# Optimization experiments

Hardware: AMD Instinct MI355X
Metric: run time of the kernel (lower is better)

The kernel has to match this reference:

```python
import jax, jax.numpy as jnp
import numpy as np

N_NODES = 100000
N_EDGES = 1600000
N_GRAPHS = 512


def gcn_conv(x, W, b, src, dst, n_nodes):
    """GCNConv with self-loops: D^-1/2 (A+I) D^-1/2 X W + b."""
    h = x @ W  # [N, out]
    ones = jnp.ones((src.shape[0],), h.dtype)
    deg = jax.ops.segment_sum(ones, dst, num_segments=n_nodes) + 1.0  # +1 self-loop
    dinv = jax.lax.rsqrt(deg)
    norm = dinv[src] * dinv[dst]  # [E]
    agg = jax.ops.segment_sum(h[src] * norm[:, None], dst, num_segments=n_nodes)
    agg = agg + h * (1.0 / deg)[:, None]  # self-loop term: deg^-0.5 * deg^-0.5
    return agg + b


def setup_inputs() -> dict:
    key = jax.random.key(0)
    ks = jax.random.split(key, 12)
    x = jax.random.normal(ks[0], (N_NODES, 78), dtype=jnp.float32)
    edge_index = jax.random.randint(ks[1], (2, N_EDGES), 0, N_NODES, dtype=jnp.int64)
    batch = jnp.sort(jax.random.randint(ks[2], (N_NODES,), 0, N_GRAPHS, dtype=jnp.int64))
    def glorot(k, shape):
        lim = np.sqrt(6.0 / (shape[0] + shape[1])).astype(np.float32)
        return jax.random.uniform(k, shape, jnp.float32, -lim, lim)
    return {
        "x": x,
        "edge_index": edge_index,
        "batch": batch,
        "W1": glorot(ks[3], (78, 128)),
        "b1": jnp.zeros((128,), jnp.float32),
        "W2": glorot(ks[4], (128, 256)),
        "b2": jnp.zeros((256,), jnp.float32),
        "Wg1": glorot(ks[5], (256, 1024)),
        "bg1": jnp.zeros((1024,), jnp.float32),
        "Wg2": glorot(ks[6], (1024, 128)),
        "bg2": jnp.zeros((128,), jnp.float32),
    }


def reference(x, edge_index, batch, W1, b1, W2, b2, Wg1, bg1, Wg2, bg2):
    src, dst = edge_index[0], edge_index[1]
    n = x.shape[0]
    h = jax.nn.relu(gcn_conv(x, W1, b1, src, dst, n))   # [N,128]
    h = jax.nn.relu(gcn_conv(h, W2, b2, src, dst, n))   # [N,256]
    g = jax.ops.segment_max(h, batch, num_segments=N_GRAPHS)  # global max pool [G,256]
    g = jax.nn.relu(g @ Wg1 + bg1)   # [G,1024]; dropout is identity at eval
    g = g @ Wg2 + bg2                # [G,128]
    return g
```

## Files before the change

kernel.cpp:

```cpp
#include <hip/hip_runtime.h>
#include <hip/hip_fp16.h>


#define NN 100000
#define NE 1600000
#define NG 512
#define NBLK ((NN + 1023) / 1024)

typedef float v2f __attribute__((ext_vector_type(2)));
typedef _Float16 half8 __attribute__((ext_vector_type(8)));
typedef float f32x4 __attribute__((ext_vector_type(4)));


__global__ void k_hist(const int* __restrict__ dst, int* cnt, int e) {
    int i = blockIdx.x * blockDim.x + threadIdx.x;
    if (i < e) atomicAdd(&cnt[dst[i]], 1);
}

__global__ void k_prep(const int* __restrict__ cnt, float* __restrict__ dinv,
                       float* __restrict__ gmax) {
    int i = blockIdx.x * blockDim.x + threadIdx.x;
    if (i < NN) dinv[i] = rsqrtf((float)cnt[i] + 1.0f);
    if (i < NG * 256) gmax[i] = 0.0f;
}

__global__ void k_cvt_x(const float* __restrict__ x, __half* __restrict__ xh) {
    int i = blockIdx.x * blockDim.x + threadIdx.x;
    if (i < NN * 39) {
        float2 v = ((const float2*)x)[i];
        ((__half2*)xh)[i] = __floats2half2_rn(v.x, v.y);
    }
}

__global__ void k_pack_w2(const float* __restrict__ W, __half* __restrict__ Wh,
                          __half* __restrict__ Wl) {
    int i = blockIdx.x * blockDim.x + threadIdx.x;
    if (i >= 32768) return;
    int j = i & 7, lane = (i >> 3) & 63, ks = (i >> 9) & 3, nt = i >> 11;
    int n = nt * 16 + (lane & 15);
    int k = ks * 32 + ((lane >> 4) << 3) + j;
    float v = W[k * 256 + n];
    __half hi = __float2half_rn(v);
    Wh[i] = hi;
    Wl[i] = __float2half_rn(v - __half2float(hi));
}

__global__ __launch_bounds__(256) void k_bsum(const int* __restrict__ cnt, int* __restrict__ bsum) {
    __shared__ int s[256];
    int b = blockIdx.x, t = threadIdx.x;
    int base = b * 1024 + t * 4;
    int v = 0;
#pragma unroll
    for (int j = 0; j < 4; j++) { int i = base + j; if (i < NN) v += cnt[i]; }
    s[t] = v; __syncthreads();
    for (int off = 128; off > 0; off >>= 1) {
        if (t < off) s[t] += s[t + off];
        __syncthreads();
    }
    if (t == 0) bsum[b] = s[0];
}

__global__ __launch_bounds__(128) void k_scan_bsum(int* bsum, int* row_ptr) {
    __shared__ int s[128];
    int t = threadIdx.x;
    int v = (t < NBLK) ? bsum[t] : 0;
    s[t] = v; __syncthreads();
    for (int off = 1; off < 128; off <<= 1) {
        int u = (t >= off) ? s[t - off] : 0;
        __syncthreads();
        s[t] += u;
        __syncthreads();
    }
    if (t < NBLK) bsum[t] = s[t] - v;
    if (t == 0) row_ptr[NN] = NE;
}

__global__ __launch_bounds__(256) void k_scan_blocks(const int* __restrict__ cnt,
    const int* __restrict__ bsum, int* __restrict__ row_ptr, int* __restrict__ cursor) {
    __shared__ int s[256];
    int b = blockIdx.x, t = threadIdx.x;
    int base = b * 1024 + t * 4;
    int v[4]; int sum = 0;
#pragma unroll
    for (int j = 0; j < 4; j++) { int i = base + j; v[j] = (i < NN) ? cnt[i] : 0; sum += v[j]; }
    s[t] = sum; __syncthreads();
    for (int off = 1; off < 256; off <<= 1) {
        int u = (t >= off) ? s[t - off] : 0;
        __syncthreads();
        s[t] += u;
        __syncthreads();
    }
    int excl = s[t] - sum + bsum[b];
#pragma unroll
    for (int j = 0; j < 4; j++) {
        int i = base + j;
        if (i < NN) { row_ptr[i] = excl; cursor[i] = excl; excl += v[j]; }
    }
}

__global__ void k_fillslots(const int* __restrict__ src, const int* __restrict__ dst,
    const float* __restrict__ dinv, int* cursor, int2* __restrict__ es, int e) {
    int i = blockIdx.x * blockDim.x + threadIdx.x;
    if (i >= e) return;
    int s = src[i], d = dst[i];
    int pos = atomicAdd(&cursor[d], 1);
    es[pos] = make_int2(s, __float_as_int(dinv[s] * dinv[d]));
}

__global__ __launch_bounds__(256) void k_fused1(const __half* __restrict__ x,
    const int* __restrict__ rp, const int2* __restrict__ es,
    const float* __restrict__ dinv, const float* __restrict__ W,
    const float* __restrict__ bias, __half* __restrict__ out) {
    __shared__ float As[4][8][80];
    int tid = threadIdx.x;
    int wv = tid >> 6, l = tid & 63;
    int task = __builtin_amdgcn_readfirstlane(blockIdx.x * 4 + wv);
    int n0 = task * 8;
    if (n0 >= NN) return;

    if (l < 39) {
        for (int pi = 0; pi < 4; pi++) {
            int nA = n0 + 2 * pi, nB = nA + 1;
            float diA = dinv[nA], swA = diA * diA;
            float diB = dinv[nB], swB = diB * diB;
            float2 aA = __half22float2(((const __half2*)(x + (size_t)nA * 78))[l]);
            float2 aB = __half22float2(((const __half2*)(x + (size_t)nB * 78))[l]);
            aA.x *= swA; aA.y *= swA;
            aB.x *= swB; aB.y *= swB;
            int eA = rp[nA], eA1 = rp[nA + 1];
            int eB = rp[nB], eB1 = rp[nB + 1];
            int cA = (eA1 - eA) >> 3, cB = (eB1 - eB) >> 3;
            while (cA > 0 || cB > 0) {
                bool dA = (cA > 0), dB = (cB > 0);
                int2 esA[8], esB[8];
                __half2 vA[8], vB[8];
                if (dA) {
#pragma unroll
                    for (int j = 0; j < 8; j++) esA[j] = es[eA + j];
                }
                if (dB) {
#pragma unroll
                    for (int j = 0; j < 8; j++) esB[j] = es[eB + j];
                }
                if (dA) {
#pragma unroll
                    for (int j = 0; j < 8; j++)
                        vA[j] = ((const __half2*)(x + (size_t)esA[j].x * 78))[l];
                }
                if (dB) {
#pragma unroll
                    for (int j = 0; j < 8; j++)
                        vB[j] = ((const __half2*)(x + (size_t)esB[j].x * 78))[l];
                }
                if (dA) {
#pragma unroll
                    for (int j = 0; j < 8; j++) {
                        float w = __int_as_float(esA[j].y);
                        float2 v = __half22float2(vA[j]);
                        aA.x += v.x * w; aA.y += v.y * w;
                    }
                    eA += 8; cA--;
                }
                if (dB) {
#pragma unroll
                    for (int j = 0; j < 8; j++) {
                        float w = __int_as_float(esB[j].y);
                        float2 v = __half22float2(vB[j]);
                        aB.x += v.x * w; aB.y += v.y * w;
                    }
                    eB += 8; cB--;
                }
            }
            while (eA < eA1 && eB < eB1) {
                int2 pA = es[eA], pB = es[eB];
                float2 vA2 = __half22float2(((const __half2*)(x + (size_t)pA.x * 78))[l]);
                float2 vB2 = __half22float2(((const __half2*)(x + (size_t)pB.x * 78))[l]);
                float wA = __int_as_float(pA.y), wB = __int_as_float(pB.y);
                aA.x += vA2.x * wA; aA.y += vA2.y * wA;
                aB.x += vB2.x * wB; aB.y += vB2.y * wB;
                eA++; eB++;
            }
            for (; eA < eA1; eA++) {
                int2 p = es[eA];
                float w = __int_as_float(p.y);
                float2 v = __half22float2(((const __half2*)(x + (size_t)p.x * 78))[l]);
                aA.x += v.x * w; aA.y += v.y * w;
            }
            for (; eB < eB1; eB++) {
                int2 p = es[eB];
                float w = __int_as_float(p.y);
                float2 v = __half22float2(((const __half2*)(x + (size_t)p.x * 78))[l]);
                aB.x += v.x * w; aB.y += v.y * w;
            }
            *(float2*)&As[wv][2 * pi][2 * l] = aA;
            *(float2*)&As[wv][2 * pi + 1][2 * l] = aB;
        }
    }

    int f0 = l * 2;
    float2 acc[8];
#pragma unroll
    for (int i = 0; i < 8; i++) acc[i] = make_float2(0.f, 0.f);

    for (int k = 0; k < 76; k += 4) {
        float2 w0 = *(const float2*)&W[(k + 0) * 128 + f0];
        float2 w1 = *(const float2*)&W[(k + 1) * 128 + f0];
        float2 w2 = *(const float2*)&W[(k + 2) * 128 + f0];
        float2 w3 = *(const float2*)&W[(k + 3) * 128 + f0];
#pragma unroll
        for (int i = 0; i < 8; i++) {
            float4 a = *(const float4*)&As[wv][i][k];
            acc[i].x += a.x * w0.x + a.y * w1.x + a.z * w2.x + a.w * w3.x;
            acc[i].y += a.x * w0.y + a.y * w1.y + a.z * w2.y + a.w * w3.y;
        }
    }
    {
        float2 w0 = *(const float2*)&W[76 * 128 + f0];
        float2 w1 = *(const float2*)&W[77 * 128 + f0];
#pragma unroll
        for (int i = 0; i < 8; i++) {
            float2 a = *(const float2*)&As[wv][i][76];
            acc[i].x += a.x * w0.x + a.y * w1.x;
            acc[i].y += a.x * w0.y + a.y * w1.y;
        }
    }
    float2 bv = *(const float2*)&bias[f0];
#pragma unroll
    for (int i = 0; i < 8; i++) {
        float ox = fmaxf(acc[i].x + bv.x, 0.f);
        float oy = fmaxf(acc[i].y + bv.y, 0.f);
        *(__half2*)&out[(size_t)(n0 + i) * 128 + f0] = __floats2half2_rn(ox, oy);
    }
}

__global__ __launch_bounds__(256) void k_fused2(const __half* __restrict__ h,
    const int* __restrict__ rp, const int2* __restrict__ es,
    const float* __restrict__ dinv, const __half* __restrict__ W2h,
    const __half* __restrict__ W2l, const float* __restrict__ bias,
    const int* __restrict__ batch, unsigned* __restrict__ gmax) {
    __shared__ __half As[4][16][128];
    int tid = threadIdx.x;
    int wv = tid >> 6, l = tid & 63;
    int task = __builtin_amdgcn_readfirstlane(blockIdx.x * 4 + wv);
    if (task >= 6250) return;
    int n0 = task * 16;

    char* lbase = (char*)&As[wv][0][0];
    int chunkw = (l >> 2);
    int subw = (l & 3) * 4;

    for (int pi = 0; pi < 8; pi++) {
        int nA = n0 + 2 * pi, nB = nA + 1;
        float diA = dinv[nA], swA = diA * diA;
        float diB = dinv[nB], swB = diB * diB;
        float2 aA = __half22float2(((const __half2*)(h + (size_t)nA * 128))[l]);
        float2 aB = __half22float2(((const __half2*)(h + (size_t)nB * 128))[l]);
        aA.x *= swA; aA.y *= swA;
        aB.x *= swB; aB.y *= swB;
        int eA = rp[nA], eA1 = rp[nA + 1];
        int eB = rp[nB], eB1 = rp[nB + 1];
        int cA = (eA1 - eA) >> 3, cB = (eB1 - eB) >> 3;
        while (cA > 0 || cB > 0) {
            bool dA = (cA > 0), dB = (cB > 0);
            int2 esA[8], esB[8];
            __half2 vA[8], vB[8];
            if (dA) {
#pragma unroll
                for (int j = 0; j < 8; j++) esA[j] = es[eA + j];
            }
            if (dB) {
#pragma unroll
                for (int j = 0; j < 8; j++) esB[j] = es[eB + j];
            }
            if (dA) {
#pragma unroll
                for (int j = 0; j < 8; j++)
                    vA[j] = ((const __half2*)(h + (size_t)esA[j].x * 128))[l];
            }
            if (dB) {
#pragma unroll
                for (int j = 0; j < 8; j++)
                    vB[j] = ((const __half2*)(h + (size_t)esB[j].x * 128))[l];
            }
            if (dA) {
#pragma unroll
                for (int j = 0; j < 8; j++) {
                    float w = __int_as_float(esA[j].y);
                    float2 v = __half22float2(vA[j]);
                    aA.x += v.x * w; aA.y += v.y * w;
                }
                eA += 8; cA--;
            }
            if (dB) {
#pragma unroll
                for (int j = 0; j < 8; j++) {
                    float w = __int_as_float(esB[j].y);
                    float2 v = __half22float2(vB[j]);
                    aB.x += v.x * w; aB.y += v.y * w;
                }
                eB += 8; cB--;
            }
        }
        while (eA < eA1 && eB < eB1) {
            int2 pA = es[eA], pB = es[eB];
            float2 vA2 = __half22float2(((const __half2*)(h + (size_t)pA.x * 128))[l]);
            float2 vB2 = __half22float2(((const __half2*)(h + (size_t)pB.x * 128))[l]);
            float wA = __int_as_float(pA.y), wB = __int_as_float(pB.y);
            aA.x += vA2.x * wA; aA.y += vA2.y * wA;
            aB.x += vB2.x * wB; aB.y += vB2.y * wB;
            eA++; eB++;
        }
        for (; eA < eA1; eA++) {
            int2 p = es[eA];
            float w = __int_as_float(p.y);
            float2 v = __half22float2(((const __half2*)(h + (size_t)p.x * 128))[l]);
            aA.x += v.x * w; aA.y += v.y * w;
        }
        for (; eB < eB1; eB++) {
            int2 p = es[eB];
            float w = __int_as_float(p.y);
            float2 v = __half22float2(((const __half2*)(h + (size_t)p.x * 128))[l]);
            aB.x += v.x * w; aB.y += v.y * w;
        }
        int rA = 2 * pi, rB = 2 * pi + 1;
        *(__half2*)(lbase + rA * 256 + ((chunkw ^ rA) << 4) + subw) =
            __floats2half2_rn(aA.x, aA.y);
        *(__half2*)(lbase + rB * 256 + ((chunkw ^ rB) << 4) + subw) =
            __floats2half2_rn(aB.x, aB.y);
    }

    int am = l & 15;
    int row4 = (l >> 4) << 2;
    int gg[4];
#pragma unroll
    for (int r = 0; r < 4; r++) gg[r] = batch[n0 + row4 + r];

    half8 ah[4];
#pragma unroll
    for (int ks = 0; ks < 4; ks++) {
        int c = ks * 4 + (l >> 4);
        ah[ks] = *(const half8*)(lbase + am * 256 + ((c ^ am) << 4));
    }

    for (int hh = 0; hh < 2; hh++) {
        f32x4 acc[8];
#pragma unroll
        for (int i = 0; i < 8; i++) acc[i] = (f32x4)(0.f);
#pragma unroll
        for (int ks = 0; ks < 4; ks++) {
#pragma unroll
            for (int nt = 0; nt < 8; nt++) {
                int fi = ((((hh * 8 + nt) * 4 + ks) * 64) + l) * 8;
                half8 bh = *(const half8*)&W2h[fi];
                half8 bl = *(const half8*)&W2l[fi];
                acc[nt] = __builtin_amdgcn_mfma_f32_16x16x32_f16(ah[ks], bh, acc[nt], 0, 0, 0);
                acc[nt] = __builtin_amdgcn_mfma_f32_16x16x32_f16(ah[ks], bl, acc[nt], 0, 0, 0);
            }
        }
#pragma unroll
        for (int nt = 0; nt < 8; nt++) {
            int n = (hh * 8 + nt) * 16 + am;
            float bv = bias[n];
            int curg = -1;
            float m = 0.f;
#pragma unroll
            for (int r = 0; r < 4; r++) {
                int g = gg[r];
                float v = fmaxf(acc[nt][r] + bv, 0.f);
                if (g != curg) {
                    if (curg >= 0) atomicMax(&gmax[(size_t)curg * 256 + n], __float_as_uint(m));
                    curg = g; m = v;
                } else {
                    m = fmaxf(m, v);
                }
            }
            if (curg >= 0) atomicMax(&gmax[(size_t)curg * 256 + n], __float_as_uint(m));
        }
    }
}


__global__ __launch_bounds__(256) void k_gemm3(const float* __restrict__ A,
    const float* __restrict__ W, const float* __restrict__ bias,
    float* __restrict__ out) {
    __shared__ float rs[8][256];
    int b = blockIdx.x, tid = threadIdx.x;
#pragma unroll
    for (int g = 0; g < 8; g++) rs[g][tid] = A[(b * 8 + g) * 256 + tid];
    __syncthreads();
    float acc[8][4];
#pragma unroll
    for (int g = 0; g < 8; g++)
#pragma unroll
        for (int j = 0; j < 4; j++) acc[g][j] = 0.f;
    for (int k = 0; k < 256; k++) {
        float w0 = W[k * 1024 + tid];
        float w1 = W[k * 1024 + tid + 256];
        float w2 = W[k * 1024 + tid + 512];
        float w3 = W[k * 1024 + tid + 768];
#pragma unroll
        for (int g = 0; g < 8; g++) {
            float a = rs[g][k];
            acc[g][0] += a * w0; acc[g][1] += a * w1;
            acc[g][2] += a * w2; acc[g][3] += a * w3;
        }
    }
#pragma unroll
    for (int g = 0; g < 8; g++)
#pragma unroll
        for (int j = 0; j < 4; j++) {
            int f = tid + j * 256;
            out[(b * 8 + g) * 1024 + f] = fmaxf(acc[g][j] + bias[f], 0.0f);
        }
}

__global__ __launch_bounds__(128) void k_gemm4(const float* __restrict__ A,
    const float* __restrict__ W, const float* __restrict__ bias,
    float* __restrict__ out) {
    __shared__ float rs[4][1024];
    int b = blockIdx.x, tid = threadIdx.x;
    for (int i = tid; i < 4096; i += 128) rs[i >> 10][i & 1023] = A[b * 4096 + i];
    __syncthreads();
    float acc[4] = {0.f, 0.f, 0.f, 0.f};
    for (int k = 0; k < 1024; k++) {
        float wv = W[k * 128 + tid];
#pragma unroll
        for (int g = 0; g < 4; g++) acc[g] += rs[g][k] * wv;
    }
#pragma unroll
    for (int g = 0; g < 4; g++)
        out[(b * 4 + g) * 128 + tid] = acc[g] + bias[tid];
}

extern "C" void kernel_launch(void* const* d_in, const int* in_sizes, int n_in,
                              void* d_out, int out_size, void* d_ws, size_t ws_size,
                              hipStream_t stream) {
    const float* x    = (const float*)d_in[0];
    const int*   ei   = (const int*)d_in[1];
    const int*   batch= (const int*)d_in[2];
    const float* W1   = (const float*)d_in[3];
    const float* b1   = (const float*)d_in[4];
    const float* W2   = (const float*)d_in[5];
    const float* b2   = (const float*)d_in[6];
    const float* Wg1  = (const float*)d_in[7];
    const float* bg1  = (const float*)d_in[8];
    const float* Wg2  = (const float*)d_in[9];
    const float* bg2  = (const float*)d_in[10];
    const int* src = ei;
    const int* dst = ei + NE;

    char* w8 = (char*)d_ws;
    int*   cnt     = (int*)w8;                 w8 += (size_t)NN * 4;
    int*   row_ptr = (int*)w8;                 w8 += (size_t)(NN + 4) * 4;
    int*   cursor  = (int*)w8;                 w8 += (size_t)NN * 4;
    int*   bsum    = (int*)w8;                 w8 += 128 * 4;
    int2*  es      = (int2*)w8;                w8 += (size_t)NE * 8;
    float* dinv    = (float*)w8;               w8 += (size_t)NN * 4;
    __half* xh     = (__half*)w8;              w8 += (size_t)NN * 78 * 2;
    __half* h1     = (__half*)w8;              w8 += (size_t)NN * 128 * 2;
    __half* w2h    = (__half*)w8;              w8 += 32768 * 2;
    __half* w2l    = (__half*)w8;              w8 += 32768 * 2;
    unsigned* gmax = (unsigned*)w8;            w8 += (size_t)NG * 256 * 4;
    float* g1      = (float*)w8;               w8 += (size_t)NG * 1024 * 4;

    hipMemsetAsync(cnt, 0, (size_t)NN * 4, stream);
    k_hist<<<(NE + 255) / 256, 256, 0, stream>>>(dst, cnt, NE);
    k_cvt_x<<<(NN * 39 + 255) / 256, 256, 0, stream>>>(x, xh);
    k_pack_w2<<<128, 256, 0, stream>>>(W2, w2h, w2l);
    k_prep<<<(NG * 256 + 255) / 256, 256, 0, stream>>>(cnt, dinv, (float*)gmax);
    k_bsum<<<NBLK, 256, 0, stream>>>(cnt, bsum);
    k_scan_bsum<<<1, 128, 0, stream>>>(bsum, row_ptr);
    k_scan_blocks<<<NBLK, 256, 0, stream>>>(cnt, bsum, row_ptr, cursor);
    k_fillslots<<<(NE + 255) / 256, 256, 0, stream>>>(src, dst, dinv, cursor, es, NE);

    k_fused1<<<NN / 32, 256, 0, stream>>>(xh, row_ptr, es, dinv, W1, b1, h1);

    k_fused2<<<(6250 + 3) / 4, 256, 0, stream>>>(h1, row_ptr, es, dinv, w2h, w2l, b2, batch, gmax);

    k_gemm3<<<NG / 8, 256, 0, stream>>>((const float*)gmax, Wg1, bg1, g1);
    k_gemm4<<<NG / 4, 128, 0, stream>>>(g1, Wg2, bg2, (float*)d_out);
}
```

Baseline: 591.1 us.

## Split layer-2 gather from MFMA pooling and degree-sort pairs in layer 1

Layer 2 is split into two kernels. The first gathers neighbour rows, one node per wavefront, with software-prefetched edge slots, and writes a half-precision aggregate buffer. The second runs the MFMA GEMM over 64-row tiles and does the max-pool epilogue. Separately, layer 1 sorts each wave's 8 nodes by degree so the paired nodes have similar edge counts, which reduces divergence in the dual-node loop. The split costs an extra write and read of a 100k x 128 half buffer. The MFMA tail tile reads padded rows of that buffer that were never written; those rows are masked out in the pooling step.

```diff
diff --git a/kernel.cpp b/kernel.cpp
--- a/kernel.cpp
+++ b/kernel.cpp
@@ -6,6 +6,8 @@
 #define NE 1600000
 #define NG 512
 #define NBLK ((NN + 1023) / 1024)
+#define NTASK2 1563
+#define NNPAD 100032
 
 typedef float v2f __attribute__((ext_vector_type(2)));
 typedef _Float16 half8 __attribute__((ext_vector_type(8)));
@@ -118,9 +120,28 @@
     int n0 = task * 8;
     if (n0 >= NN) return;
 
+    int deg[8], idx[8];
+    {
+        int e0 = rp[n0], ei;
+#pragma unroll
+        for (int i = 0; i < 8; i++) {
+            ei = rp[n0 + i + 1];
+            deg[i] = ei - e0; e0 = ei; idx[i] = i;
+        }
+    }
+#pragma unroll
+    for (int i = 1; i < 8; i++) {
+        int dv = deg[i], iv = idx[i], j = i - 1;
+        while (j >= 0 && deg[j] > dv) {
+            deg[j + 1] = deg[j]; idx[j + 1] = idx[j]; j--;
+        }
+        deg[j + 1] = dv; idx[j + 1] = iv;
+    }
+
     if (l < 39) {
         for (int pi = 0; pi < 4; pi++) {
-            int nA = n0 + 2 * pi, nB = nA + 1;
+            int iA = idx[2 * pi], iB = idx[2 * pi + 1];
+            int nA = n0 + iA, nB = n0 + iB;
             float diA = dinv[nA], swA = diA * diA;
             float diB = dinv[nB], swB = diB * diB;
             float2 aA = __half22float2(((const __half2*)(x + (size_t)nA * 78))[l]);
@@ -192,8 +213,8 @@
                 float2 v = __half22float2(((const __half2*)(x + (size_t)p.x * 78))[l]);
                 aB.x += v.x * w; aB.y += v.y * w;
             }
-            *(float2*)&As[wv][2 * pi][2 * l] = aA;
-            *(float2*)&As[wv][2 * pi + 1][2 * l] = aB;
+            *(float2*)&As[wv][iA][2 * l] = aA;
+            *(float2*)&As[wv][iB][2 * l] = aB;
         }
     }
 
@@ -233,148 +254,113 @@
     }
 }
 
-__global__ __launch_bounds__(256) void k_fused2(const __half* __restrict__ h,
+__global__ __launch_bounds__(256) void k_gather128h(const __half* __restrict__ h,
     const int* __restrict__ rp, const int2* __restrict__ es,
-    const float* __restrict__ dinv, const __half* __restrict__ W2h,
-    const __half* __restrict__ W2l, const float* __restrict__ bias,
-    const int* __restrict__ batch, unsigned* __restrict__ gmax) {
-    __shared__ __half As[4][16][128];
+    const float* __restrict__ dinv, __half* __restrict__ agg) {
+    int n = blockIdx.x * 4 + (threadIdx.x >> 6);
+    int l = threadIdx.x & 63;
+    float di = dinv[n], sw = di * di;
+    float2 a = __half22float2(((const __half2*)(h + (size_t)n * 128))[l]);
+    a.x *= sw; a.y *= sw;
+    int e = rp[n], e1 = rp[n + 1];
+    int nf = (e1 - e) >> 3;
+    if (nf > 0) {
+        int2 cur[8];
+#pragma unroll
+        for (int j = 0; j < 8; j++) cur[j] = es[e + j];
+        for (int b = 1; ; b++) {
+            __half2 v[8];
+#pragma unroll
+            for (int j = 0; j < 8; j++)
+                v[j] = ((const __half2*)(h + (size_t)cur[j].x * 128))[l];
+            e += 8;
+            bool more = (b < nf);
+            int2 nxt[8];
+            if (more) {
+#pragma unroll
+                for (int j = 0; j < 8; j++) nxt[j] = es[e + j];
+            }
+#pragma unroll
+            for (int j = 0; j < 8; j++) {
+                float w = __int_as_float(cur[j].y);
+                float2 vv = __half22float2(v[j]);
+                a.x += vv.x * w; a.y += vv.y * w;
+            }
+            if (!more) break;
+#pragma unroll
+            for (int j = 0; j < 8; j++) cur[j] = nxt[j];
+        }
+    }
+    for (; e < e1; e++) {
+        int2 p = es[e];
+        float w = __int_as_float(p.y);
+        float2 v = __half22float2(((const __half2*)(h + (size_t)p.x * 128))[l]);
+        a.x += v.x * w; a.y += v.y * w;
+    }
+    ((__half2*)(agg + (size_t)n * 128))[l] = __floats2half2_rn(a.x, a.y);
+}
+
+__global__ __launch_bounds__(256) void k_mm2pool(const __half* __restrict__ A,
+    const __half* __restrict__ W2h, const __half* __restrict__ W2l,
+    const float* __restrict__ bias, const int* __restrict__ batch,
+    unsigned* __restrict__ gmax) {
     int tid = threadIdx.x;
     int wv = tid >> 6, l = tid & 63;
     int task = __builtin_amdgcn_readfirstlane(blockIdx.x * 4 + wv);
-    if (task >= 6250) return;
-    int n0 = task * 16;
-
-    char* lbase = (char*)&As[wv][0][0];
-    int chunkw = (l >> 2);
-    int subw = (l & 3) * 4;
-
-    for (int pi = 0; pi < 8; pi++) {
-        int nA = n0 + 2 * pi, nB = nA + 1;
-        float diA = dinv[nA], swA = diA * diA;
-        float diB = dinv[nB], swB = diB * diB;
-        float2 aA = __half22float2(((const __half2*)(h + (size_t)nA * 128))[l]);
-        float2 aB = __half22float2(((const __half2*)(h + (size_t)nB * 128))[l]);
-        aA.x *= swA; aA.y *= swA;
-        aB.x *= swB; aB.y *= swB;
-        int eA = rp[nA], eA1 = rp[nA + 1];
-        int eB = rp[nB], eB1 = rp[nB + 1];
-        int cA = (eA1 - eA) >> 3, cB = (eB1 - eB) >> 3;
-        while (cA > 0 || cB > 0) {
-            bool dA = (cA > 0), dB = (cB > 0);
-            int2 esA[8], esB[8];
-            __half2 vA[8], vB[8];
-            if (dA) {
-#pragma unroll
-                for (int j = 0; j < 8; j++) esA[j] = es[eA + j];
-            }
-            if (dB) {
-#pragma unroll
-                for (int j = 0; j < 8; j++) esB[j] = es[eB + j];
-            }
-            if (dA) {
-#pragma unroll
-                for (int j = 0; j < 8; j++)
-                    vA[j] = ((const __half2*)(h + (size_t)esA[j].x * 128))[l];
-            }
-            if (dB) {
-#pragma unroll
-                for (int j = 0; j < 8; j++)
-                    vB[j] = ((const __half2*)(h + (size_t)esB[j].x * 128))[l];
-            }
-            if (dA) {
-#pragma unroll
-                for (int j = 0; j < 8; j++) {
-                    float w = __int_as_float(esA[j].y);
-                    float2 v = __half22float2(vA[j]);
-                    aA.x += v.x * w; aA.y += v.y * w;
-                }
-                eA += 8; cA--;
-            }
-            if (dB) {
-#pragma unroll
-                for (int j = 0; j < 8; j++) {
-                    float w = __int_as_float(esB[j].y);
-                    float2 v = __half22float2(vB[j]);
-                    aB.x += v.x * w; aB.y += v.y * w;
-                }
-                eB += 8; cB--;
-            }
-        }
-        while (eA < eA1 && eB < eB1) {
-            int2 pA = es[eA], pB = es[eB];
-            float2 vA2 = __half22float2(((const __half2*)(h + (size_t)pA.x * 128))[l]);
-            float2 vB2 = __half22float2(((const __half2*)(h + (size_t)pB.x * 128))[l]);
-            float wA = __int_as_float(pA.y), wB = __int_as_float(pB.y);
-            aA.x += vA2.x * wA; aA.y += vA2.y * wA;
-            aB.x += vB2.x * wB; aB.y += vB2.y * wB;
-            eA++; eB++;
-        }
-        for (; eA < eA1; eA++) {
-            int2 p = es[eA];
-            float w = __int_as_float(p.y);
-            float2 v = __half22float2(((const __half2*)(h + (size_t)p.x * 128))[l]);
-            aA.x += v.x * w; aA.y += v.y * w;
-        }
-        for (; eB < eB1; eB++) {
-            int2 p = es[eB];
-            float w = __int_as_float(p.y);
-            float2 v = __half22float2(((const __half2*)(h + (size_t)p.x * 128))[l]);
-            aB.x += v.x * w; aB.y += v.y * w;
-        }
-        int rA = 2 * pi, rB = 2 * pi + 1;
-        *(__half2*)(lbase + rA * 256 + ((chunkw ^ rA) << 4) + subw) =
-            __floats2half2_rn(aA.x, aA.y);
-        *(__half2*)(lbase + rB * 256 + ((chunkw ^ rB) << 4) + subw) =
-            __floats2half2_rn(aB.x, aB.y);
-    }
-
+    if (task >= NTASK2) return;
+    int n0 = task * 64;
     int am = l & 15;
     int row4 = (l >> 4) << 2;
-    int gg[4];
-#pragma unroll
-    for (int r = 0; r < 4; r++) gg[r] = batch[n0 + row4 + r];
-
-    half8 ah[4];
-#pragma unroll
-    for (int ks = 0; ks < 4; ks++) {
-        int c = ks * 4 + (l >> 4);
-        ah[ks] = *(const half8*)(lbase + am * 256 + ((c ^ am) << 4));
-    }
+    int kb = (l >> 4) << 3;
+
+    half8 ah[4][4];
+#pragma unroll
+    for (int t = 0; t < 4; t++)
+#pragma unroll
+        for (int ks = 0; ks < 4; ks++)
+            ah[t][ks] = *(const half8*)&A[(size_t)(n0 + t * 16 + am) * 128 + ks * 32 + kb];
 
     for (int hh = 0; hh < 2; hh++) {
-        f32x4 acc[8];
-#pragma unroll
-        for (int i = 0; i < 8; i++) acc[i] = (f32x4)(0.f);
-#pragma unroll
-        for (int ks = 0; ks < 4; ks++) {
-#pragma unroll
-            for (int nt = 0; nt < 8; nt++) {
+#pragma unroll
+        for (int nt = 0; nt < 8; nt++) {
+            f32x4 acc[4];
+#pragma unroll
+            for (int t = 0; t < 4; t++) acc[t] = (f32x4)(0.f);
+#pragma unroll
+            for (int ks = 0; ks < 4; ks++) {
                 int fi = ((((hh * 8 + nt) * 4 + ks) * 64) + l) * 8;
                 half8 bh = *(const half8*)&W2h[fi];
                 half8 bl = *(const half8*)&W2l[fi];
-                acc[nt] = __builtin_amdgcn_mfma_f32_16x16x32_f16(ah[ks], bh, acc[nt], 0, 0, 0);
-                acc[nt] = __builtin_amdgcn_mfma_f32_16x16x32_f16(ah[ks], bl, acc[nt], 0, 0, 0);
-            }
-        }
-#pragma unroll
-        for (int nt = 0; nt < 8; nt++) {
-            int n = (hh * 8 + nt) * 16 + am;
-            float bv = bias[n];
+#pragma unroll
+                for (int t = 0; t < 4; t++) {
+                    acc[t] = __builtin_amdgcn_mfma_f32_16x16x32_f16(ah[t][ks], bh, acc[t], 0, 0, 0);
+                    acc[t] = __builtin_amdgcn_mfma_f32_16x16x32_f16(ah[t][ks], bl, acc[t], 0, 0, 0);
+                }
+            }
+            int ncol = (hh * 8 + nt) * 16 + am;
+            float bv = bias[ncol];
             int curg = -1;
             float m = 0.f;
 #pragma unroll
-            for (int r = 0; r < 4; r++) {
-                int g = gg[r];
-                float v = fmaxf(acc[nt][r] + bv, 0.f);
-                if (g != curg) {
-                    if (curg >= 0) atomicMax(&gmax[(size_t)curg * 256 + n], __float_as_uint(m));
-                    curg = g; m = v;
-                } else {
-                    m = fmaxf(m, v);
-                }
-            }
-            if (curg >= 0) atomicMax(&gmax[(size_t)curg * 256 + n], __float_as_uint(m));
+            for (int t = 0; t < 4; t++) {
+#pragma unroll
+                for (int r = 0; r < 4; r++) {
+                    int node = n0 + t * 16 + row4 + r;
+                    if (node < NN) {
+                        int g = batch[node];
+                        float v = fmaxf(acc[t][r] + bv, 0.f);
+                        if (g != curg) {
+                            if (curg >= 0)
+                                atomicMax(&gmax[(size_t)curg * 256 + ncol], __float_as_uint(m));
+                            curg = g; m = v;
+                        } else {
+                            m = fmaxf(m, v);
+                        }
+                    }
+                }
+            }
+            if (curg >= 0)
+                atomicMax(&gmax[(size_t)curg * 256 + ncol], __float_as_uint(m));
         }
     }
 }
@@ -458,6 +444,7 @@
     float* dinv    = (float*)w8;               w8 += (size_t)NN * 4;
     __half* xh     = (__half*)w8;              w8 += (size_t)NN * 78 * 2;
     __half* h1     = (__half*)w8;              w8 += (size_t)NN * 128 * 2;
+    __half* agg2   = (__half*)w8;              w8 += (size_t)NNPAD * 128 * 2;
     __half* w2h    = (__half*)w8;              w8 += 32768 * 2;
     __half* w2l    = (__half*)w8;              w8 += 32768 * 2;
     unsigned* gmax = (unsigned*)w8;            w8 += (size_t)NG * 256 * 4;
@@ -475,7 +462,8 @@
 
     k_fused1<<<NN / 32, 256, 0, stream>>>(xh, row_ptr, es, dinv, W1, b1, h1);
 
-    k_fused2<<<(6250 + 3) / 4, 256, 0, stream>>>(h1, row_ptr, es, dinv, w2h, w2l, b2, batch, gmax);
+    k_gather128h<<<NN / 4, 256, 0, stream>>>(h1, row_ptr, es, dinv, agg2);
+    k_mm2pool<<<(NTASK2 + 3) / 4, 256, 0, stream>>>(agg2, w2h, w2l, b2, batch, gmax);
 
     k_gemm3<<<NG / 8, 256, 0, stream>>>((const float*)gmax, Wg1, bg1, g1);
     k_gemm4<<<NG / 4, 128, 0, stream>>>(g1, Wg2, bg2, (float*)d_out);
```

New measurement: 598.7 us. Within noise of the previous version (+1.3%).
